# Performance work log

Hardware: AMD Instinct MI355X
Metric: run time of the kernel (lower is better)

Reference implementation:

```python
import jax, jax.numpy as jnp
import numpy as np
from jax import lax

H, W = 1024, 2048
WIN = (3, 3)            # eps=1.5 on the integer grid == 8-neighborhood (3x3 window)
MIN_SAMPLES = 4         # sklearn DBSCAN counts the point itself
MIN_CLUSTER = 30        # clusters smaller than this become noise
N_SLOTS = 26            # output channels
INT32_MAX = np.iinfo(np.int32).max


def setup_inputs() -> dict:
    key = jax.random.key(0)
    mask = jax.random.normal(key, (H, W), dtype=jnp.float32)
    return {"mask": mask}


def _minpool(x):
    # 3x3 min over int32 labels, SAME padding with +inf identity
    return lax.reduce_window(x, INT32_MAX, lax.min, WIN, (1, 1), 'SAME')


def _forward(mask):
    h, w = mask.shape
    hw = h * w
    BIG = jnp.int32(hw)  # sentinel label for 'not in any cluster'

    active = mask > 0.1
    # neighbor count in 3x3 (includes self) -> DBSCAN core condition
    cnt = lax.reduce_window(active.astype(jnp.int32), 0, lax.add, WIN, (1, 1), 'SAME')
    core = active & (cnt >= MIN_SAMPLES)

    idx2d = jnp.arange(hw, dtype=jnp.int32).reshape(h, w)
    L0 = jnp.where(core, idx2d, BIG)

    # connected components over core pixels: min-label hook (3x3 min-pool)
    # + pointer jumping (path compression) until fixpoint
    def body(st):
        L, _ = st
        Ln = jnp.where(core, jnp.minimum(L, _minpool(L)), BIG)
        flat = Ln.ravel()
        table = jnp.concatenate([flat, jnp.array([hw], jnp.int32)])  # BIG -> BIG
        flat = table[table[flat]]  # two pointer-jump hops
        Ln = flat.reshape(h, w)
        return Ln, jnp.all(Ln == L)

    def cond(st):
        return jnp.logical_not(st[1])

    L, _ = lax.while_loop(cond, body, (L0, jnp.array(False)))

    # border points: active non-core pixels with a core neighbor join the
    # (deterministically min-labeled) neighboring core cluster
    pooled = _minpool(L)
    final = jnp.where(core, L, jnp.where(active & (pooled < BIG), pooled, BIG))

    flatL = final.ravel()
    labeled = flatL < BIG
    ids = jnp.where(labeled, flatL, hw)  # noise -> extra bucket hw

    sizes = jax.ops.segment_sum(labeled.astype(jnp.int32), ids, num_segments=hw + 1)[:hw]
    col = jnp.broadcast_to(jnp.arange(w, dtype=jnp.float32), (h, w)).ravel()
    colsum = jax.ops.segment_sum(jnp.where(labeled, col, 0.0), ids, num_segments=hw + 1)[:hw]

    valid = sizes >= MIN_CLUSTER  # size filter (loc.sum() < 30 -> noise)
    means = jnp.where(valid, colsum / jnp.maximum(sizes, 1), jnp.inf)
    order = jnp.argsort(means)  # valid clusters first, sorted by mean column
    rank = jnp.zeros(hw, jnp.int32).at[order].set(jnp.arange(hw, dtype=jnp.int32))

    lab = jnp.where(labeled, flatL, 0)
    ch = rank[lab]
    pix_ok = labeled & valid[lab] & (ch < N_SLOTS)
    ch2d = jnp.where(pix_ok, ch, N_SLOTS).reshape(h, w)  # N_SLOTS == 'no channel'
    # scatter 1s into the rank-th channel
    return (ch2d[None] == jnp.arange(N_SLOTS, dtype=jnp.int32)[:, None, None]).astype(jnp.uint8)


def reference(mask):
    return _forward(mask)
```

## Files before the change

### kernel.cpp

```cpp
#include <hip/hip_runtime.h>
#include <stdint.h>

#define HH 1024
#define WW 2048
#define HWN (HH*WW)
#define BIGL HWN
#define NSLOTS 26
#define MINCL 30
#define THREADS 256
#define LTHREADS 512
#define MAXCAND 70000
#define HSZ 512
#define TILE 4096
#define NTILES 512
#define NB 128

typedef int vi4 __attribute__((ext_vector_type(4)));
typedef unsigned long long u64;

__device__ __forceinline__ int uf_load(int* p, int i) {
    return __hip_atomic_load(&p[i], __ATOMIC_RELAXED, __HIP_MEMORY_SCOPE_AGENT);
}
__device__ __forceinline__ void uf_store(int* p, int i, int v) {
    __hip_atomic_store(&p[i], v, __ATOMIC_RELAXED, __HIP_MEMORY_SCOPE_AGENT);
}
__device__ int uf_find(int* parent, int x) {
    int p = uf_load(parent, x);
    while (p != x) {
        int gp = uf_load(parent, p);
        if (gp != p) uf_store(parent, x, gp);
        x = p; p = gp;
    }
    return p;
}
__device__ void uf_union(int* parent, int a, int b) {
    int ra = uf_find(parent, a);
    int rb = uf_find(parent, b);
    while (ra != rb) {
        if (ra > rb) { int t = ra; ra = rb; rb = t; }
        int old = atomicCAS(&parent[rb], rb, ra);
        if (old == rb) return;
        rb = uf_find(parent, old);
        ra = uf_find(parent, ra);
    }
}

__device__ __forceinline__ int l_load(int* p, int i) {
    return __hip_atomic_load(&p[i], __ATOMIC_RELAXED, __HIP_MEMORY_SCOPE_WORKGROUP);
}
__device__ __forceinline__ void l_store(int* p, int i, int v) {
    __hip_atomic_store(&p[i], v, __ATOMIC_RELAXED, __HIP_MEMORY_SCOPE_WORKGROUP);
}
__device__ int l_find(int* lp, int x) {
    int p = l_load(lp, x);
    while (p != x) {
        int gp = l_load(lp, p);
        if (gp != p) l_store(lp, x, gp);
        x = p; p = gp;
    }
    return p;
}
__device__ void l_union(int* lp, int a, int b) {
    int ra = l_find(lp, a);
    int rb = l_find(lp, b);
    while (ra != rb) {
        if (ra > rb) { int t = ra; ra = rb; rb = t; }
        int old = atomicCAS(&lp[rb], rb, ra);
        if (old == rb) return;
        rb = l_find(lp, old);
        ra = l_find(lp, ra);
    }
}

__global__ __launch_bounds__(LTHREADS) void k_local(const float* __restrict__ mask,
                                                    uint8_t* __restrict__ flags,
                                                    int* __restrict__ parent,
                                                    int* __restrict__ sizes,
                                                    unsigned long long* __restrict__ colsum,
                                                    signed char* __restrict__ chan,
                                                    int* __restrict__ counter) {
    __shared__ uint8_t lact[66 * 72];
    __shared__ uint8_t lc8[TILE];
    __shared__ int lp[TILE];
    const int tid = threadIdx.x;
    int tile_x = blockIdx.x & 31, tile_y = blockIdx.x >> 5;
    int r0 = tile_y << 6, c0 = tile_x << 6;

    {
        int base = blockIdx.x * (HWN / NTILES);
        vi4* sz4 = (vi4*)(sizes + base);
        vi4* cs4 = (vi4*)(colsum + base);
        for (int t = tid; t < 1024; t += LTHREADS) sz4[t] = (vi4)0;
        for (int t = tid; t < 2048; t += LTHREADS) cs4[t] = (vi4)0;
        vi4* ch4 = (vi4*)(chan + base);
        for (int t = tid; t < 256; t += LTHREADS) ch4[t] = (vi4)(-1);
        if (blockIdx.x == 0 && tid == 0) { counter[0] = 0; counter[1] = 0; }
    }

    {
        int lr = tid >> 4, q = tid & 15;
        #pragma unroll
        for (int pass = 0; pass < 2; ++pass) {
            int rr = lr + pass * 32;
            const float4* src = (const float4*)(mask + (size_t)(r0 + rr) * WW + c0);
            float4 v = src[q];
            uint8_t* dst = &lact[(rr + 1) * 72 + (q * 4 + 1)];
            dst[0] = v.x > 0.1f; dst[1] = v.y > 0.1f;
            dst[2] = v.z > 0.1f; dst[3] = v.w > 0.1f;
        }
    }
    if (tid < 32) {
        int q = tid & 15;
        bool top = tid < 16;
        int gr = top ? r0 - 1 : r0 + 64;
        int yy = top ? 0 : 65;
        uint8_t* dst = &lact[yy * 72 + (q * 4 + 1)];
        if ((unsigned)gr < HH) {
            const float4* src = (const float4*)(mask + (size_t)gr * WW + c0);
            float4 v = src[q];
            dst[0] = v.x > 0.1f; dst[1] = v.y > 0.1f;
            dst[2] = v.z > 0.1f; dst[3] = v.w > 0.1f;
        } else {
            dst[0] = 0; dst[1] = 0; dst[2] = 0; dst[3] = 0;
        }
    } else if (tid >= 64 && tid < 64 + 132) {
        int lane = tid - 64;
        int side = lane >= 66;
        int yy = side ? lane - 66 : lane;
        int gr = r0 - 1 + yy;
        int gc = side ? c0 + 64 : c0 - 1;
        bool a = false;
        if ((unsigned)gr < HH && (unsigned)gc < WW) a = mask[(size_t)gr * WW + gc] > 0.1f;
        lact[yy * 72 + (side ? 65 : 0)] = a ? 1 : 0;
    }
    __syncthreads();
    for (int li = tid; li < TILE; li += LTHREADS) {
        int lr = li >> 6, lc = li & 63;
        int b = (lr + 1) * 72 + (lc + 1);
        int a = lact[b];
        int cnt = lact[b - 73] + lact[b - 72] + lact[b - 71]
                + lact[b - 1]  + a           + lact[b + 1]
                + lact[b + 71] + lact[b + 72] + lact[b + 73];
        lc8[li] = (uint8_t)(a | ((a && cnt >= 4) ? 2 : 0));
        lp[li] = li;
    }
    __syncthreads();
    if (tid < 256) {
        int row = tid >> 2, chunk = tid & 3;
        ((uint4*)(flags + (size_t)(r0 + row) * WW + c0))[chunk] =
            ((const uint4*)lc8)[row * 4 + chunk];
    }
    for (int li = tid; li < TILE; li += LTHREADS) {
        if (!(lc8[li] & 2)) continue;
        int lr = li >> 6, lc = li & 63;
        if (lc > 0 && (lc8[li - 1] & 2)) l_union(lp, li, li - 1);
        if (lr > 0) {
            if (lc > 0  && (lc8[li - 65] & 2)) l_union(lp, li, li - 65);
            if (           (lc8[li - 64] & 2)) l_union(lp, li, li - 64);
            if (lc < 63 && (lc8[li - 63] & 2)) l_union(lp, li, li - 63);
        }
    }
    __syncthreads();
    for (int li = tid; li < TILE; li += LTHREADS) {
        if (!(lc8[li] & 2)) continue;
        int root = li, p;
        while ((p = lp[root]) != root) root = p;
        int gi = (r0 + (li >> 6)) * WW + c0 + (li & 63);
        int gr = (r0 + (root >> 6)) * WW + c0 + (root & 63);
        parent[gi] = gr;
    }
}

__global__ __launch_bounds__(THREADS) void k_merge(const uint8_t* __restrict__ flags,
                                                   int* __restrict__ parent) {
    int tile_x = blockIdx.x & 31, tile_y = blockIdx.x >> 5;
    int r0 = tile_y << 6, c0 = tile_x << 6;
    int t = threadIdx.x;
    int lane = t & 63;

    if (t < 64) {
        int r = r0, c = c0 + t, i = r * WW + c;
        bool selfC = (flags[i] & 2) != 0;
        bool nC = false, nwC = false, neC = false;
        if (selfC && r > 0) {
            nC  = (flags[i - WW] & 2) != 0;
            nwC = (c > 0)      && (flags[i - WW - 1] & 2);
            neC = (c < WW - 1) && (flags[i - WW + 1] & 2);
        }
        int did = 0, ra = -1, rb = -1;
        if (selfC && r > 0 && nC) { ra = uf_find(parent, i); rb = uf_find(parent, i - WW); did = 1; }
        int pra = __shfl_up(ra, 1), prb = __shfl_up(rb, 1), pdid = __shfl_up(did, 1);
        bool head = (lane == 0) || !pdid || pra != ra || prb != rb;
        if (did && head) uf_union(parent, ra, rb);
        if (selfC && r > 0) {
            if (t == 0) {
                if (nwC) uf_union(parent, i, i - WW - 1);
                if (!nC && neC) uf_union(parent, i, i - WW + 1);
            } else if (t == 63) {
                if (!nC && nwC) uf_union(parent, i, i - WW - 1);
                if (neC) {
                    bool eC = (c < WW - 1) && (flags[i + 1] & 2);
                    if (!eC) uf_union(parent, i, i - WW + 1);
                }
            } else if (!nC) {
                if (nwC) uf_union(parent, i, i - WW - 1);
                if (neC) uf_union(parent, i, i - WW + 1);
            }
        }
        if (t == 0 && selfC && c > 0 && (flags[i - 1] & 2))
            uf_union(parent, i, i - 1);
    } else if (t < 127) {
        int lr = t - 63;
        int r = r0 + lr, c = c0, i = r * WW + c;
        bool selfC = (flags[i] & 2) != 0;
        bool wC = false, nwC = false;
        if (selfC && c > 0) {
            wC  = (flags[i - 1] & 2) != 0;
            nwC = (flags[i - WW - 1] & 2) != 0;
        }
        int did = 0, ra = -1, rb = -1;
        if (selfC && wC) { ra = uf_find(parent, i); rb = uf_find(parent, i - 1); did = 1; }
        int pra = __shfl_up(ra, 1), prb = __shfl_up(rb, 1), pdid = __shfl_up(did, 1);
        bool head = (lane == 0) || !pdid || pra != ra || prb != rb;
        if (did && head) uf_union(parent, ra, rb);
        if (selfC && !wC && nwC) uf_union(parent, i, i - WW - 1);
    } else if (t < 190) {
        int lr = t - 126;
        int r = r0 + lr, c = c0 + 63, i = r * WW + c;
        bool selfC = (flags[i] & 2) != 0;
        if (selfC && c < WW - 1) {
            bool neC = (flags[i - WW + 1] & 2) != 0;
            bool eC  = (flags[i + 1] & 2) != 0;
            if (neC && !eC) uf_union(parent, i, i - WW + 1);
        }
    }
}

__device__ __forceinline__ void h_insert(int* h_key, int p) {
    unsigned slot = (((unsigned)p * 2654435761u) >> 20) & (HSZ - 1);
    for (;;) {
        int old = atomicCAS(&h_key[slot], -1, p);
        if (old == -1 || old == p) return;
        slot = (slot + 1) & (HSZ - 1);
    }
}
__device__ __forceinline__ int h_lookup(const int* h_key, const int* h_root, int p) {
    unsigned slot = (((unsigned)p * 2654435761u) >> 20) & (HSZ - 1);
    for (;;) {
        if (h_key[slot] == p) return h_root[slot];
        slot = (slot + 1) & (HSZ - 1);
    }
}

__global__ __launch_bounds__(THREADS) void k_border_stats(
        const uint8_t* __restrict__ flags, int* __restrict__ parent,
        int* __restrict__ labfull, int* __restrict__ sizes,
        unsigned long long* __restrict__ colsum,
        int* __restrict__ cand, int* __restrict__ counter) {
    __shared__ int h_key[HSZ];
    __shared__ int h_root[HSZ];
    __shared__ int s_lab[HSZ];
    __shared__ int s_sz[HSZ];
    __shared__ u64 s_cs[HSZ];
    for (int t = threadIdx.x; t < HSZ; t += THREADS) {
        h_key[t] = -1; s_lab[t] = -1; s_sz[t] = 0; s_cs[t] = 0;
    }
    __syncthreads();

    const int i = blockIdx.x * THREADS + threadIdx.x;
    const int f = flags[i];
    const int r = i >> 11, c = i & (WW - 1);

    int pself = -1;
    int pnb[8];
    #pragma unroll
    for (int t = 0; t < 8; ++t) pnb[t] = -1;

    if (f & 2) {
        pself = parent[i];
        h_insert(h_key, pself);
    } else if (f & 1) {
        const int dr8[8] = {-1,-1,-1, 0,0, 1,1,1};
        const int dc8[8] = {-1, 0, 1,-1,1,-1,0,1};
        #pragma unroll
        for (int t = 0; t < 8; ++t) {
            int rr = r + dr8[t], cc = c + dc8[t];
            if ((unsigned)rr < HH && (unsigned)cc < WW) {
                int n = rr * WW + cc;
                if (flags[n] & 2) {
                    int p = parent[n];
                    pnb[t] = p;
                    h_insert(h_key, p);
                }
            }
        }
    }
    __syncthreads();
    for (int t = threadIdx.x; t < HSZ; t += THREADS) {
        int k = h_key[t];
        if (k >= 0) h_root[t] = uf_find(parent, k);
    }
    __syncthreads();

    int lab = BIGL;
    if (f & 2) {
        lab = h_lookup(h_key, h_root, pself);
    } else if (f & 1) {
        int m = BIGL;
        #pragma unroll
        for (int t = 0; t < 8; ++t)
            if (pnb[t] >= 0) { int v = h_lookup(h_key, h_root, pnb[t]); if (v < m) m = v; }
        lab = m;
    }
    labfull[i] = lab;

    int lane = threadIdx.x & 63;
    int labp = __shfl_up(lab, 1);
    bool head = (lane == 0) || (labp != lab);
    unsigned long long hm = __ballot(head);
    if (head && lab < BIGL) {
        unsigned long long rest = (hm >> lane) >> 1;
        int len = rest ? __ffsll((unsigned long long)rest) : (64 - lane);
        long long cc0 = (long long)(i & (WW - 1));
        u64 csum = (u64)(cc0 * len + (long long)len * (len - 1) / 2);
        unsigned slot = (((unsigned)lab * 2654435761u) >> 20) & (HSZ - 1);
        for (;;) {
            int old = atomicCAS(&s_lab[slot], -1, lab);
            if (old == -1 || old == lab) {
                atomicAdd(&s_sz[slot], len);
                atomicAdd(&s_cs[slot], csum);
                break;
            }
            slot = (slot + 1) & (HSZ - 1);
        }
    }
    __syncthreads();
    for (int t = threadIdx.x; t < HSZ; t += THREADS) {
        int lb = s_lab[t];
        if (lb >= 0) {
            int add = s_sz[t];
            int old = atomicAdd(&sizes[lb], add);
            if (old < MINCL && old + add >= MINCL) {
                int p = atomicAdd(counter, 1);
                cand[p] = lb;
            }
            atomicAdd(&colsum[lb], s_cs[t]);
        }
    }
}

__device__ __forceinline__ u64 wave_min_u64(u64 m) {
    #pragma unroll
    for (int off = 32; off; off >>= 1) {
        u64 o = __shfl_xor(m, off);
        if (o < m) m = o;
    }
    return m;
}

__global__ __launch_bounds__(THREADS) void k_sel(const int* __restrict__ cand,
                                                 int* __restrict__ counter,
                                                 const int* __restrict__ sizes,
                                                 const unsigned long long* __restrict__ colsum,
                                                 unsigned long long* __restrict__ top26g,
                                                 signed char* __restrict__ chan) {
    __shared__ u64 wout[4 * NSLOTS];
    const int tid = threadIdx.x, lane = tid & 63, wv = tid >> 6;
    const int n = counter[0];
    int slice = (n + NB - 1) / NB;
    int j0 = blockIdx.x * slice;
    int j1 = j0 + slice; if (j1 > n) j1 = n;
    int len = j1 - j0; if (len < 0) len = 0;
    int chunk = (len + 3) >> 2;
    int s0 = j0 + wv * chunk;
    int s1 = s0 + chunk; if (s1 > j1) s1 = j1;

    u64 kk[3] = { ~0ull, ~0ull, ~0ull };
    #pragma unroll
    for (int t = 0; t < 3; ++t) {
        int j = s0 + lane + 64 * t;
        if (j < s1) {
            int lab = cand[j];
            float mean = (float)colsum[lab] / (float)sizes[lab];
            kk[t] = ((u64)__float_as_uint(mean) << 32) | (unsigned)lab;
        }
    }
    for (int k = 0; k < NSLOTS; ++k) {
        u64 m = kk[0]; int li = 0;
        if (kk[1] < m) { m = kk[1]; li = 1; }
        if (kk[2] < m) { m = kk[2]; li = 2; }
        u64 mpre = m;
        m = wave_min_u64(m);
        if (mpre == m && m != ~0ull) kk[li] = ~0ull;
        if (lane == 0) wout[wv * NSLOTS + k] = m;
    }
    __syncthreads();
    if (wv == 0) {
        u64 a = (lane < 4 * NSLOTS) ? wout[lane] : ~0ull;
        u64 b = (lane + 64 < 4 * NSLOTS) ? wout[lane + 64] : ~0ull;
        for (int k = 0; k < NSLOTS; ++k) {
            u64 m = a < b ? a : b; int li = a < b ? 0 : 1;
            u64 mpre = m;
            m = wave_min_u64(m);
            if (mpre == m && m != ~0ull) { if (li == 0) a = ~0ull; else b = ~0ull; }
            if (lane == 0) top26g[blockIdx.x * NSLOTS + k] = m;
        }
    }
    __syncthreads();
    __shared__ int lastflag;
    if (tid == 0) {
        __threadfence();
        lastflag = (atomicAdd(&counter[1], 1) == NB - 1);
    }
    __syncthreads();
    if (!lastflag) return;

    u64 mk[13];
    #pragma unroll
    for (int t = 0; t < 13; ++t) {
        int j = wv * 832 + lane + 64 * t;
        mk[t] = __hip_atomic_load(&top26g[j], __ATOMIC_RELAXED, __HIP_MEMORY_SCOPE_AGENT);
    }
    for (int k = 0; k < NSLOTS; ++k) {
        u64 m = mk[0]; int li = 0;
        #pragma unroll
        for (int t = 1; t < 13; ++t) if (mk[t] < m) { m = mk[t]; li = t; }
        u64 mpre = m;
        m = wave_min_u64(m);
        if (mpre == m && m != ~0ull) mk[li] = ~0ull;
        if (lane == 0) wout[wv * NSLOTS + k] = m;
    }
    __syncthreads();
    if (wv == 0) {
        u64 a = (lane < 4 * NSLOTS) ? wout[lane] : ~0ull;
        u64 b = (lane + 64 < 4 * NSLOTS) ? wout[lane + 64] : ~0ull;
        for (int k = 0; k < NSLOTS; ++k) {
            u64 m = a < b ? a : b; int li = a < b ? 0 : 1;
            u64 mpre = m;
            m = wave_min_u64(m);
            if (mpre == m && m != ~0ull) { if (li == 0) a = ~0ull; else b = ~0ull; }
            if (lane == 0 && m != ~0ull)
                chan[(unsigned int)(m & 0xFFFFFFFFull)] = (signed char)k;
        }
    }
}

__global__ __launch_bounds__(THREADS) void k_output(const int* __restrict__ labfull,
                                                    const signed char* __restrict__ chan,
                                                    int* __restrict__ out) {
    int i4 = (blockIdx.x * THREADS + threadIdx.x) * 4;
    int chv[4];
    #pragma unroll
    for (int t = 0; t < 4; ++t) {
        int lab = labfull[i4 + t];
        chv[t] = (lab < BIGL) ? (int)chan[lab] : -1;
    }
    #pragma unroll
    for (int c = 0; c < NSLOTS; ++c) {
        vi4 v;
        v.x = (chv[0] == c) ? 1 : 0;
        v.y = (chv[1] == c) ? 1 : 0;
        v.z = (chv[2] == c) ? 1 : 0;
        v.w = (chv[3] == c) ? 1 : 0;
        __builtin_nontemporal_store(v, (vi4*)(out + (size_t)c * HWN + i4));
    }
}

extern "C" void kernel_launch(void* const* d_in, const int* in_sizes, int n_in,
                              void* d_out, int out_size, void* d_ws, size_t ws_size,
                              hipStream_t stream) {
    const float* mask = (const float*)d_in[0];
    int* out = (int*)d_out;

    char* w = (char*)d_ws;
    int* parent                 = (int*)(w);
    int* labfull                = (int*)(w + (size_t)HWN * 4);
    int* sizes                  = (int*)(w + (size_t)HWN * 8);
    unsigned long long* colsum  = (unsigned long long*)(w + (size_t)HWN * 12);
    uint8_t* flags              = (uint8_t*)(w + (size_t)HWN * 20);
    signed char* chan           = (signed char*)(w + (size_t)HWN * 21);
    int* cand                   = (int*)(w + (size_t)HWN * 22);
    int* counter                = (int*)(w + (size_t)HWN * 22 + MAXCAND * 4);
    unsigned long long* top26g  = (unsigned long long*)(w + (size_t)HWN * 22 + MAXCAND * 4 + 256);

    const int blocks = HWN / THREADS;
    k_local       <<<NTILES, LTHREADS, 0, stream>>>(mask, flags, parent,
                                                    sizes, colsum, chan, counter);
    k_merge       <<<NTILES, THREADS, 0, stream>>>(flags, parent);
    k_border_stats<<<blocks, THREADS, 0, stream>>>(flags, parent, labfull, sizes, colsum,
                                                   cand, counter);
    k_sel         <<<NB, THREADS, 0, stream>>>(cand, counter, sizes, colsum, top26g, chan);
    k_output      <<<HWN / (4 * THREADS), THREADS, 0, stream>>>(labfull, chan, out);
}
```

Measured before the change: 388.1 us.

## Recompute labels in output kernel instead of storing labfull; prune redundant local unions

The border/stats kernel no longer writes an 8 MB per-pixel label array. The output kernel instead recomputes each pixel's label from flags and parent, using a 2048-entry shared hash table and union-find lookups. Separately, the local tile union step skips neighbor unions already implied by the north or west neighbor, using the 8-connectivity decision-tree trick. This trades a full write plus read of labfull for redundant neighbor gathers and find operations in the output kernel, which raises shared-memory use and may lower occupancy.

```diff
diff --git a/kernel.cpp b/kernel.cpp
--- a/kernel.cpp
+++ b/kernel.cpp
@@ -11,6 +11,7 @@
 #define LTHREADS 512
 #define MAXCAND 70000
 #define HSZ 512
+#define HSZ2 2048
 #define TILE 4096
 #define NTILES 512
 #define NB 128
@@ -153,11 +154,17 @@
     for (int li = tid; li < TILE; li += LTHREADS) {
         if (!(lc8[li] & 2)) continue;
         int lr = li >> 6, lc = li & 63;
-        if (lc > 0 && (lc8[li - 1] & 2)) l_union(lp, li, li - 1);
+        bool w = (lc > 0) && (lc8[li - 1] & 2);
+        if (w) l_union(lp, li, li - 1);
         if (lr > 0) {
-            if (lc > 0  && (lc8[li - 65] & 2)) l_union(lp, li, li - 65);
-            if (           (lc8[li - 64] & 2)) l_union(lp, li, li - 64);
-            if (lc < 63 && (lc8[li - 63] & 2)) l_union(lp, li, li - 63);
+            bool n = (lc8[li - 64] & 2) != 0;
+            if (n) {
+                l_union(lp, li, li - 64);
+            } else {
+                if (!w && lc > 0 && (lc8[li - 65] & 2)) l_union(lp, li, li - 65);
+                if (lc < 63 && !(lc8[li + 1] & 2) && (lc8[li - 63] & 2))
+                    l_union(lp, li, li - 63);
+            }
         }
     }
     __syncthreads();
@@ -254,8 +261,7 @@
 
 __global__ __launch_bounds__(THREADS) void k_border_stats(
         const uint8_t* __restrict__ flags, int* __restrict__ parent,
-        int* __restrict__ labfull, int* __restrict__ sizes,
-        unsigned long long* __restrict__ colsum,
+        int* __restrict__ sizes, unsigned long long* __restrict__ colsum,
         int* __restrict__ cand, int* __restrict__ counter) {
     __shared__ int h_key[HSZ];
     __shared__ int h_root[HSZ];
@@ -312,7 +318,6 @@
             if (pnb[t] >= 0) { int v = h_lookup(h_key, h_root, pnb[t]); if (v < m) m = v; }
         lab = m;
     }
-    labfull[i] = lab;
 
     int lane = threadIdx.x & 63;
     int labp = __shfl_up(lab, 1);
@@ -445,14 +450,78 @@
     }
 }
 
-__global__ __launch_bounds__(THREADS) void k_output(const int* __restrict__ labfull,
+__device__ __forceinline__ void h2_insert(int* hk, int p) {
+    unsigned slot = (((unsigned)p * 2654435761u) >> 16) & (HSZ2 - 1);
+    for (;;) {
+        int old = atomicCAS(&hk[slot], -1, p);
+        if (old == -1 || old == p) return;
+        slot = (slot + 1) & (HSZ2 - 1);
+    }
+}
+__device__ __forceinline__ int h2_lookup(const int* hk, const int* hr, int p) {
+    unsigned slot = (((unsigned)p * 2654435761u) >> 16) & (HSZ2 - 1);
+    for (;;) {
+        if (hk[slot] == p) return hr[slot];
+        slot = (slot + 1) & (HSZ2 - 1);
+    }
+}
+
+__global__ __launch_bounds__(THREADS) void k_output(const uint8_t* __restrict__ flags,
+                                                    int* __restrict__ parent,
                                                     const signed char* __restrict__ chan,
                                                     int* __restrict__ out) {
-    int i4 = (blockIdx.x * THREADS + threadIdx.x) * 4;
+    __shared__ int hk[HSZ2];
+    __shared__ int hr[HSZ2];
+    for (int t = threadIdx.x; t < HSZ2; t += THREADS) hk[t] = -1;
+    __syncthreads();
+    const int i4 = (blockIdx.x * THREADS + threadIdx.x) * 4;
+    uchar4 f4 = *(const uchar4*)(flags + i4);
+    vi4 p4 = *(const vi4*)(parent + i4);
+    const uint8_t ff[4] = { f4.x, f4.y, f4.z, f4.w };
+    const int pv[4] = { p4.x, p4.y, p4.z, p4.w };
+    int pnb[4][8];
+    const int dr8[8] = {-1,-1,-1, 0,0, 1,1,1};
+    const int dc8[8] = {-1, 0, 1,-1,1,-1,0,1};
+    #pragma unroll
+    for (int t = 0; t < 4; ++t) {
+        #pragma unroll
+        for (int e = 0; e < 8; ++e) pnb[t][e] = -1;
+        int f = ff[t];
+        if (f & 2) {
+            h2_insert(hk, pv[t]);
+        } else if (f & 1) {
+            int i = i4 + t;
+            int r = i >> 11, c = i & (WW - 1);
+            #pragma unroll
+            for (int e = 0; e < 8; ++e) {
+                int rr = r + dr8[e], cc = c + dc8[e];
+                if ((unsigned)rr < HH && (unsigned)cc < WW) {
+                    int n = rr * WW + cc;
+                    if (flags[n] & 2) { int p = parent[n]; pnb[t][e] = p; h2_insert(hk, p); }
+                }
+            }
+        }
+    }
+    __syncthreads();
+    for (int t = threadIdx.x; t < HSZ2; t += THREADS) {
+        int k = hk[t];
+        if (k >= 0) hr[t] = uf_find(parent, k);
+    }
+    __syncthreads();
     int chv[4];
     #pragma unroll
     for (int t = 0; t < 4; ++t) {
-        int lab = labfull[i4 + t];
+        int f = ff[t];
+        int lab = BIGL;
+        if (f & 2) {
+            lab = h2_lookup(hk, hr, pv[t]);
+        } else if (f & 1) {
+            int m = BIGL;
+            #pragma unroll
+            for (int e = 0; e < 8; ++e)
+                if (pnb[t][e] >= 0) { int v = h2_lookup(hk, hr, pnb[t][e]); if (v < m) m = v; }
+            lab = m;
+        }
         chv[t] = (lab < BIGL) ? (int)chan[lab] : -1;
     }
     #pragma unroll
@@ -474,7 +543,6 @@
 
     char* w = (char*)d_ws;
     int* parent                 = (int*)(w);
-    int* labfull                = (int*)(w + (size_t)HWN * 4);
     int* sizes                  = (int*)(w + (size_t)HWN * 8);
     unsigned long long* colsum  = (unsigned long long*)(w + (size_t)HWN * 12);
     uint8_t* flags              = (uint8_t*)(w + (size_t)HWN * 20);
@@ -487,8 +555,8 @@
     k_local       <<<NTILES, LTHREADS, 0, stream>>>(mask, flags, parent,
                                                     sizes, colsum, chan, counter);
     k_merge       <<<NTILES, THREADS, 0, stream>>>(flags, parent);
-    k_border_stats<<<blocks, THREADS, 0, stream>>>(flags, parent, labfull, sizes, colsum,
+    k_border_stats<<<blocks, THREADS, 0, stream>>>(flags, parent, sizes, colsum,
                                                    cand, counter);
     k_sel         <<<NB, THREADS, 0, stream>>>(cand, counter, sizes, colsum, top26g, chan);
-    k_output      <<<HWN / (4 * THREADS), THREADS, 0, stream>>>(labfull, chan, out);
-}
+    k_output      <<<HWN / (4 * THREADS), THREADS, 0, stream>>>(flags, parent, chan, out);
+}
```

Result: slower. 406.4 us (+4.7%).
